# Performance work log

Hardware: AMD Instinct MI355X
Metric: run time of the kernel (lower is better)

The kernel has to match this reference:

```python
import jax, jax.numpy as jnp
import numpy as np

GOP = 4


def conv3x3(x, w, b):
    y = jax.lax.conv_general_dilated(x, w, (1, 1), 'SAME',
                                     dimension_numbers=('NCHW', 'OIHW', 'NCHW'))
    return y + b[None, :, None, None]


def resize_bilinear(x, oh, ow):
    # F.interpolate(mode='bilinear', align_corners=False), no antialias
    N, C, H, W = x.shape
    ys = (jnp.arange(oh, dtype=x.dtype) + 0.5) * (H / oh) - 0.5
    xs = (jnp.arange(ow, dtype=x.dtype) + 0.5) * (W / ow) - 0.5
    y0 = jnp.floor(ys); x0 = jnp.floor(xs)
    ty = (ys - y0)[:, None]; tx = (xs - x0)[None, :]
    y0i = jnp.clip(y0, 0, H - 1).astype(jnp.int32)
    y1i = jnp.clip(y0 + 1, 0, H - 1).astype(jnp.int32)
    x0i = jnp.clip(x0, 0, W - 1).astype(jnp.int32)
    x1i = jnp.clip(x0 + 1, 0, W - 1).astype(jnp.int32)
    r00 = x[:, :, y0i][:, :, :, x0i]; r01 = x[:, :, y0i][:, :, :, x1i]
    r10 = x[:, :, y1i][:, :, :, x0i]; r11 = x[:, :, y1i][:, :, :, x1i]
    top = r00 * (1 - tx) + r01 * tx
    bot = r10 * (1 - tx) + r11 * tx
    return top * (1 - ty) + bot * ty


def deform_sample_1x1(feat, off):
    # torchvision deform_conv2d with 1x1 kernel: bilinear gather at
    # (h + dy, w + dx), zero outside; offset channels are (dy, dx).
    N, C, H, W = feat.shape
    dy, dx = off[:, 0], off[:, 1]                       # [N,H,W]
    gy = jnp.arange(H, dtype=feat.dtype)[:, None] + dy  # [N,H,W]
    gx = jnp.arange(W, dtype=feat.dtype)[None, :] + dx
    y0 = jnp.floor(gy); x0 = jnp.floor(gx)
    ty = (gy - y0)[:, None]; tx = (gx - x0)[:, None]    # [N,1,H,W]

    def corner(yi, xi):
        valid = (yi >= 0) & (yi < H) & (xi >= 0) & (xi < W)
        yc = jnp.clip(yi, 0, H - 1).astype(jnp.int32)
        xc = jnp.clip(xi, 0, W - 1).astype(jnp.int32)
        v = jax.vmap(lambda f, y, x: f[:, y, x])(feat, yc, xc)  # [N,C,H,W]
        return v * valid[:, None].astype(feat.dtype)

    return (corner(y0, x0) * (1 - ty) * (1 - tx)
            + corner(y0, x0 + 1) * (1 - ty) * tx
            + corner(y0 + 1, x0) * ty * (1 - tx)
            + corner(y0 + 1, x0 + 1) * ty * tx)


def setup_inputs() -> dict:
    key = jax.random.key(0)
    ks = jax.random.split(key, 20)
    dim = 256
    f32 = jnp.float32

    def p(k, shape, s=0.05):
        return jax.random.normal(k, shape, dtype=f32) * s

    return {
        'imgs': jax.random.normal(ks[0], (2, 16, 3, 224, 224), dtype=f32),
        'i_features': jax.random.normal(ks[1], (8, dim, 56, 56), dtype=f32),
        'p_motions': jax.random.normal(ks[2], (2, 12, 2, 112, 112), dtype=f32),
        'dw': p(ks[3], (dim, dim)), 'db': p(ks[4], (dim,)),
        'mw1': p(ks[5], (dim, dim, 3, 3)), 'mb1': p(ks[6], (dim,)),
        'mw2': p(ks[7], (dim, dim, 3, 3)), 'mb2': p(ks[8], (dim,)),
        'mw3': p(ks[9], (dim, dim, 3, 3)), 'mb3': p(ks[10], (dim,)),
        'ew1': p(ks[11], (dim, 2, 3, 3)), 'eb1': p(ks[12], (dim,)),
        'ew2': p(ks[13], (dim, dim, 3, 3)), 'eb2': p(ks[14], (dim,)),
        'ew3': p(ks[15], (dim, dim, 3, 3)), 'eb3': p(ks[16], (dim,)),
        'ew4': p(ks[17], (dim, dim, 3, 3)), 'eb4': p(ks[18], (dim,)),
    }


def reference(imgs, i_features, p_motions, dw, db, mw1, mb1, mw2, mb2, mw3, mb3,
              ew1, eb1, ew2, eb2, ew3, eb3, ew4, eb4):
    B = imgs.shape[0]
    num_gop = imgs.shape[1] // GOP
    h, w = i_features.shape[-2], i_features.shape[-1]
    scale = h / imgs.shape[-1]  # static python float
    Tp = p_motions.shape[1]
    k = Tp // num_gop

    # flatten motions over (b t), resize to feature res, rescale magnitudes
    pm = p_motions.reshape(B * Tp, 2, p_motions.shape[-2], p_motions.shape[-1])
    pm = resize_bilinear(pm, h, w) * scale              # [(b n k), 2, h, w]

    emb = jax.nn.relu(conv3x3(pm, ew1, eb1))
    emb = jax.nn.relu(conv3x3(emb, ew2, eb2))
    emb = jax.nn.relu(conv3x3(emb, ew3, eb3))
    emb = jax.nn.relu(conv3x3(emb, ew4, eb4))

    # i_features expanded to one copy per P-frame: (b n) -> (b n k)
    feat = jnp.repeat(i_features, k, axis=0)
    sampled = deform_sample_1x1(feat, pm)
    pf = jnp.einsum('nchw,oc->nohw', sampled, dw) + db[None, :, None, None]

    pf = jax.nn.relu(conv3x3(pf, mw1, mb1))
    pf = jax.nn.relu(conv3x3(pf, mw2, mb2))
    pf = jax.nn.relu(conv3x3(pf, mw3, mb3))
    p2d = pf + emb                                      # [(b n k), c, h, w]

    # adaptive_avg_pool2d(1) + flatten(3)
    pooled = p2d.reshape(B, num_gop, k, -1, h, w).mean(axis=(-2, -1))  # [b,n,k,c]
    return pooled, p2d
```

## Files before the change

### kernel.cpp

```cpp
#include <hip/hip_runtime.h>

#define NPIX 3136
#define NN   24
#define CDIM 256

typedef __attribute__((ext_vector_type(8))) short short8v;
typedef __attribute__((ext_vector_type(4))) float float4v;

typedef __attribute__((address_space(1))) const void gvoid;
typedef __attribute__((address_space(3))) void lvoid;
static __device__ __forceinline__ void async_copy16(const void* g, void* l) {
    __builtin_amdgcn_global_load_lds((gvoid*)g, (lvoid*)l, 16, 0, 0);
}

static __device__ __forceinline__ unsigned short f2b(float f) {
    unsigned int u = __float_as_uint(f);
    u = (u + 0x7FFFu + ((u >> 16) & 1u)) >> 16;
    return (unsigned short)u;
}
static __device__ __forceinline__ float b2f(unsigned short h) {
    return __uint_as_float(((unsigned int)h) << 16);
}

__global__ __launch_bounds__(256) void resize_pm_kernel(
    const float* __restrict__ pmo, float* __restrict__ pm)
{
    int idx = blockIdx.x * 256 + threadIdx.x;
    if (idx >= NN * 2 * NPIX) return;
    int x = idx % 56, y = (idx / 56) % 56, nc = idx / NPIX;
    const float* src = pmo + (size_t)nc * 112 * 112 + (size_t)(2 * y) * 112 + 2 * x;
    pm[idx] = (src[0] + src[1] + src[112] + src[113]) * 0.0625f;
}

__global__ __launch_bounds__(256) void pack_all_kernel(
    const float* __restrict__ s0, const float* __restrict__ s1,
    const float* __restrict__ s2, const float* __restrict__ s3,
    const float* __restrict__ s4, const float* __restrict__ s5,
    const float* __restrict__ sdw, unsigned short* __restrict__ dstbase)
{
    int bx = blockIdx.x;
    if (bx < 6 * 2304) {
        int wi = bx / 2304;
        int d = (bx % 2304) * 256 + threadIdx.x;
        const float* w = (wi == 0) ? s0 : (wi == 1) ? s1 : (wi == 2) ? s2
                       : (wi == 3) ? s3 : (wi == 4) ? s4 : s5;
        int j = d & 7;
        int lane = (d >> 3) & 63;
        int co, ci, tap;
        if (wi == 5) {
            int g = (d >> 9) & 3;
            int e = d >> 11;
            tap = e % 9;
            int f = e / 9;
            int ch = f & 7, cb = f >> 3;
            co = cb * 64 + g * 16 + (lane & 15);
            ci = ch * 32 + (lane >> 4) * 8 + j;
        } else {
            int mi = (d >> 9) & 7;
            int e = d >> 12;
            tap = e % 9;
            int f = e / 9;
            int ch = f & 7, cb = f >> 3;
            co = cb * 128 + mi * 16 + (lane & 15);
            ci = ch * 32 + (lane >> 4) * 8 + j;
        }
        dstbase[(size_t)wi * 589824 + d] = f2b(w[((size_t)co * 256 + ci) * 9 + tap]);
    } else {
        int d = (bx - 6 * 2304) * 256 + threadIdx.x;
        int j = d & 7;
        int lane = (d >> 3) & 63;
        int mi = (d >> 9) & 7;
        int e = d >> 12;
        int ch = e & 7, cb = e >> 3;
        int co = cb * 128 + mi * 16 + (lane & 15);
        int ci = ch * 32 + (lane >> 4) * 8 + j;
        dstbase[(size_t)6 * 589824 + d] = f2b(sdw[(size_t)co * 256 + ci]);
    }
}

__global__ __launch_bounds__(256) void ew1_kernel(
    const float* __restrict__ pm, const float* __restrict__ w,
    const float* __restrict__ b, unsigned short* __restrict__ out)
{
    __shared__ float sT[8][18];
    __shared__ float sW1[256 * 19];
    int n = blockIdx.y;
    int pixbase = blockIdx.x * 8;
    int t = threadIdx.x;
    if (t < 144) {
        int p = t / 18, j = t % 18;
        int ci = j / 9, tap = j % 9;
        int pix = pixbase + p;
        int y = pix / 56, x = pix % 56;
        int yy = y + tap / 3 - 1, xx = x + tap % 3 - 1;
        float v = 0.f;
        if ((unsigned)yy < 56u && (unsigned)xx < 56u)
            v = pm[((size_t)n * 2 + ci) * NPIX + yy * 56 + xx];
        sT[p][j] = v;
    }
    for (int idx = t; idx < 4608; idx += 256) {
        int co = idx / 18, j = idx % 18;
        sW1[co * 19 + j] = w[idx];
    }
    __syncthreads();
    int co = t;
    float bias = b[co];
#pragma unroll
    for (int p = 0; p < 8; p++) {
        float acc = bias;
#pragma unroll
        for (int j = 0; j < 18; j++) acc += sT[p][j] * sW1[co * 19 + j];
        acc = fmaxf(acc, 0.f);
        out[((size_t)n * NPIX + pixbase + p) * 256 + co] = f2b(acc);
    }
}

template <int TAPS, bool RELU, bool HASB>
__global__ __launch_bounds__(512, 2) void conv8_mfma(
    const unsigned short* __restrict__ in,
    const unsigned short* __restrict__ wp,
    const float* __restrict__ bias,
    unsigned short* __restrict__ out,
    const unsigned short* __restrict__ inB,
    const unsigned short* __restrict__ wpB,
    const float* __restrict__ biasB,
    unsigned short* __restrict__ outB,
    int zsplit)
{
    constexpr int W_ITERS = TAPS * 8;
    constexpr int SIN_SHORTS = (TAPS == 9) ? 10 * 58 * 32 : 448 * 32;

    __shared__ unsigned short sIn[2 * SIN_SHORTS];
    __shared__ unsigned short sW[W_ITERS * 512];

    const int r0 = blockIdx.x * 8;
    if (r0 >= 56) return;
    const int tid = threadIdx.x;
    const int lane = tid & 63;
    const int wv = tid >> 6;
    const int mih = wv >> 2;
    const int wpx = wv & 3;
    const int col = lane & 15;
    const int quad = lane >> 4;
    const int cb = blockIdx.y;

    int n = blockIdx.z;
    const unsigned short* inP = in;
    const unsigned short* wpP = wp;
    const float* biasP = bias;
    unsigned short* outP = out;
    if (n >= zsplit) {
        n -= zsplit;
        inP = inB; wpP = wpB; biasP = biasB; outP = outB;
    }

    const unsigned short* inN = inP + (size_t)n * NPIX * 256;
    const unsigned short* wcb = wpP + (size_t)cb * 8 * W_ITERS * 512;

    int rowoff[7];
#pragma unroll
    for (int nj = 0; nj < 7; nj++) {
        int pxl = wpx * 112 + nj * 16 + col;
        if (TAPS == 9) {
            int yl = pxl / 56;
            rowoff[nj] = yl * 58 + (pxl - yl * 56);
        } else {
            rowoff[nj] = pxl;
        }
    }
    const int qoff = quad * 8;
    const int laneSrc = (lane >> 2) * 256 + (lane & 3) * 8;

    auto stageW = [&](int ch) {
        const unsigned short* wchunk = wcb + (size_t)ch * W_ITERS * 512;
#pragma unroll
        for (int it = wv; it < W_ITERS; it += 8)
            async_copy16(wchunk + it * 512 + lane * 8, sW + it * 512);
    };
    auto stageI = [&](int ch, int half) {
        const int c0 = ch * 32;
        unsigned short* dst = sIn + half * SIN_SHORTS;
        if (TAPS == 9) {
#pragma unroll
            for (int s = wv; s < 40; s += 8) {
                int ry = s >> 2, k = s & 3;
                int gy = r0 + ry - 1;
                if ((unsigned)gy < 56u && (k < 3 || lane < 32))
                    async_copy16(inN + (size_t)gy * 14336 + k * 4096 + c0 + laneSrc,
                                 dst + ry * 1856 + 32 + k * 512);
            }
        } else {
#pragma unroll
            for (int s = wv; s < 28; s += 8)
                async_copy16(inN + (size_t)r0 * 14336 + s * 4096 + c0 + laneSrc,
                             dst + s * 512);
        }
    };

    if (TAPS == 9) {
        for (int i = tid * 8; i < 2 * SIN_SHORTS; i += 512 * 8)
            *(int4*)(sIn + i) = (int4){0, 0, 0, 0};
        __syncthreads();
    }

    float4v acc[4][7];
#pragma unroll
    for (int mi = 0; mi < 4; mi++)
#pragma unroll
        for (int nj = 0; nj < 7; nj++) acc[mi][nj] = (float4v){0.f, 0.f, 0.f, 0.f};

    stageW(0);
    stageI(0, 0);

    for (int ch = 0; ch < 8; ch++) {
        __syncthreads();
        if (ch < 7) stageI(ch + 1, (ch + 1) & 1);
        const int iOff = (ch & 1) * SIN_SHORTS;
#pragma unroll
        for (int tap = 0; tap < TAPS; tap++) {
            const int coff = (TAPS == 9) ? ((tap / 3) * 58 + (tap % 3)) * 32 : 0;
            short8v a[4], b[7];
#pragma unroll
            for (int mi = 0; mi < 4; mi++)
                a[mi] = *(const short8v*)(sW + ((tap * 8 + mih * 4 + mi) * 64 + lane) * 8);
#pragma unroll
            for (int nj = 0; nj < 7; nj++)
                b[nj] = *(const short8v*)(sIn + iOff + rowoff[nj] * 32 + coff + qoff);
#pragma unroll
            for (int mi = 0; mi < 4; mi++)
#pragma unroll
                for (int nj = 0; nj < 7; nj++)
                    acc[mi][nj] = __builtin_amdgcn_mfma_f32_16x16x32_bf16(
                        a[mi], b[nj], acc[mi][nj], 0, 0, 0);
        }
        if (ch < 7) {
            __syncthreads();
            stageW(ch + 1);
        }
    }

    unsigned short* outT = outP + ((size_t)n * NPIX + r0 * 56 + wpx * 112) * 256
                         + cb * 128 + mih * 64;
#pragma unroll
    for (int mi = 0; mi < 4; mi++) {
        float4v bv = (float4v){0.f, 0.f, 0.f, 0.f};
        if (HASB) bv = *(const float4v*)(biasP + cb * 128 + mih * 64 + mi * 16 + quad * 4);
#pragma unroll
        for (int nj = 0; nj < 7; nj++) {
            float v0 = acc[mi][nj][0] + bv[0];
            float v1 = acc[mi][nj][1] + bv[1];
            float v2 = acc[mi][nj][2] + bv[2];
            float v3 = acc[mi][nj][3] + bv[3];
            if (RELU) {
                v0 = fmaxf(v0, 0.f); v1 = fmaxf(v1, 0.f);
                v2 = fmaxf(v2, 0.f); v3 = fmaxf(v3, 0.f);
            }
            uint2 pk;
            pk.x = (unsigned)f2b(v0) | ((unsigned)f2b(v1) << 16);
            pk.y = (unsigned)f2b(v2) | ((unsigned)f2b(v3) << 16);
            *(uint2*)(outT + ((size_t)(nj * 16 + col)) * 256 + mi * 16 + quad * 4) = pk;
        }
    }
}

template <int TAPS, bool RELU, bool HASB, bool FUSE>
__global__ __launch_bounds__(256, 2) void conv_mfma(
    const unsigned short* __restrict__ in,
    const unsigned short* __restrict__ wp,
    const float* __restrict__ bias,
    unsigned short* __restrict__ out,
    const unsigned short* __restrict__ inB,
    const unsigned short* __restrict__ wpB,
    const float* __restrict__ biasB,
    unsigned short* __restrict__ outB,
    int zsplit,
    const unsigned short* __restrict__ emb,
    float* __restrict__ dout)
{
    constexpr int W_ITERS = TAPS * 4;
    constexpr int SIN_SHORTS = (TAPS == 9) ? 10 * 58 * 32 : 448 * 32;

    __shared__ unsigned short sIn[SIN_SHORTS];
    __shared__ unsigned short sW[W_ITERS * 512];

    const int r0 = blockIdx.x * 8;
    if (r0 >= 56) return;
    const int tid = threadIdx.x;
    const int lane = tid & 63;
    const int wv = tid >> 6;
    const int col = lane & 15;
    const int quad = lane >> 4;
    const int cb = blockIdx.y;

    int n = blockIdx.z;
    const unsigned short* inP = in;
    const unsigned short* wpP = wp;
    const float* biasP = bias;
    unsigned short* outP = out;
    if (n >= zsplit) {
        n -= zsplit;
        inP = inB; wpP = wpB; biasP = biasB; outP = outB;
    }

    const unsigned short* inN = inP + (size_t)n * NPIX * 256;
    const unsigned short* wcb = wpP + (size_t)cb * 8 * W_ITERS * 512;

    int rowoff[7];
#pragma unroll
    for (int nj = 0; nj < 7; nj++) {
        int pxl = wv * 112 + nj * 16 + col;
        if (TAPS == 9) {
            int yl = pxl / 56;
            rowoff[nj] = yl * 58 + (pxl - yl * 56);
        } else {
            rowoff[nj] = pxl;
        }
    }
    const int qoff = quad * 8;
    const int laneSrc = (lane >> 2) * 256 + (lane & 3) * 8;

    if (TAPS == 9) {
        for (int i = tid * 8; i < SIN_SHORTS; i += 2048)
            *(int4*)(sIn + i) = (int4){0, 0, 0, 0};
    }

    float4v acc[4][7];
#pragma unroll
    for (int mi = 0; mi < 4; mi++)
#pragma unroll
        for (int nj = 0; nj < 7; nj++) acc[mi][nj] = (float4v){0.f, 0.f, 0.f, 0.f};

    for (int ch = 0; ch < 8; ch++) {
        const int c0 = ch * 32;
        __syncthreads();
        const unsigned short* wchunk = wcb + (size_t)ch * W_ITERS * 512;
#pragma unroll
        for (int it = wv; it < W_ITERS; it += 4)
            async_copy16(wchunk + it * 512 + lane * 8, sW + it * 512);
        if (TAPS == 9) {
#pragma unroll
            for (int ry = 0; ry < 10; ry++) {
                int k = (wv - ry) & 3;
                int gy = r0 + ry - 1;
                if ((unsigned)gy < 56u && (k < 3 || lane < 32))
                    async_copy16(inN + (size_t)gy * 14336 + k * 4096 + c0 + laneSrc,
                                 sIn + ry * 1856 + 32 + k * 512);
            }
        } else {
#pragma unroll
            for (int k = 0; k < 7; k++) {
                int it = wv + k * 4;
                async_copy16(inN + (size_t)r0 * 14336 + it * 4096 + c0 + laneSrc,
                             sIn + it * 512);
            }
        }
        __syncthreads();
#pragma unroll
        for (int tap = 0; tap < TAPS; tap++) {
            const int coff = (TAPS == 9) ? ((tap / 3) * 58 + (tap % 3)) * 32 : 0;
            short8v a[4], b[7];
#pragma unroll
            for (int mi = 0; mi < 4; mi++)
                a[mi] = *(const short8v*)(sW + ((tap * 4 + mi) * 64 + lane) * 8);
#pragma unroll
            for (int nj = 0; nj < 7; nj++)
                b[nj] = *(const short8v*)(sIn + rowoff[nj] * 32 + coff + qoff);
#pragma unroll
            for (int mi = 0; mi < 4; mi++)
#pragma unroll
                for (int nj = 0; nj < 7; nj++)
                    acc[mi][nj] = __builtin_amdgcn_mfma_f32_16x16x32_bf16(
                        a[mi], b[nj], acc[mi][nj], 0, 0, 0);
        }
    }

    if (!FUSE) {
        unsigned short* outT = outP + ((size_t)n * NPIX + r0 * 56 + wv * 112) * 256 + cb * 64;
#pragma unroll
        for (int mi = 0; mi < 4; mi++) {
            float4v bv = (float4v){0.f, 0.f, 0.f, 0.f};
            if (HASB) bv = *(const float4v*)(biasP + cb * 64 + mi * 16 + quad * 4);
#pragma unroll
            for (int nj = 0; nj < 7; nj++) {
                float v0 = acc[mi][nj][0] + bv[0];
                float v1 = acc[mi][nj][1] + bv[1];
                float v2 = acc[mi][nj][2] + bv[2];
                float v3 = acc[mi][nj][3] + bv[3];
                if (RELU) {
                    v0 = fmaxf(v0, 0.f); v1 = fmaxf(v1, 0.f);
                    v2 = fmaxf(v2, 0.f); v3 = fmaxf(v3, 0.f);
                }
                uint2 pk;
                pk.x = (unsigned)f2b(v0) | ((unsigned)f2b(v1) << 16);
                pk.y = (unsigned)f2b(v2) | ((unsigned)f2b(v3) << 16);
                *(uint2*)(outT + ((size_t)(nj * 16 + col)) * 256 + mi * 16 + quad * 4) = pk;
            }
        }
    } else {
        const int pixBase = r0 * 56 + wv * 112;
        float* p2d = dout + 6144 + (size_t)n * CDIM * NPIX;
        float sums[4][4];
#pragma unroll
        for (int mi = 0; mi < 4; mi++)
#pragma unroll
            for (int q = 0; q < 4; q++) sums[mi][q] = 0.f;
#pragma unroll
        for (int mi = 0; mi < 4; mi++) {
            float4v bv = *(const float4v*)(biasP + cb * 64 + mi * 16 + quad * 4);
            const int co0 = cb * 64 + mi * 16 + quad * 4;
#pragma unroll
            for (int nj = 0; nj < 7; nj++) {
                int pix = pixBase + nj * 16 + col;
                uint2 e = *(const uint2*)(emb + ((size_t)n * NPIX + pix) * 256 + co0);
                float v0 = fmaxf(acc[mi][nj][0] + bv[0], 0.f) + b2f((unsigned short)(e.x & 0xFFFF));
                float v1 = fmaxf(acc[mi][nj][1] + bv[1], 0.f) + b2f((unsigned short)(e.x >> 16));
                float v2 = fmaxf(acc[mi][nj][2] + bv[2], 0.f) + b2f((unsigned short)(e.y & 0xFFFF));
                float v3 = fmaxf(acc[mi][nj][3] + bv[3], 0.f) + b2f((unsigned short)(e.y >> 16));
                p2d[(size_t)(co0 + 0) * NPIX + pix] = v0;
                p2d[(size_t)(co0 + 1) * NPIX + pix] = v1;
                p2d[(size_t)(co0 + 2) * NPIX + pix] = v2;
                p2d[(size_t)(co0 + 3) * NPIX + pix] = v3;
                sums[mi][0] += v0; sums[mi][1] += v1;
                sums[mi][2] += v2; sums[mi][3] += v3;
            }
        }
#pragma unroll
        for (int mi = 0; mi < 4; mi++)
#pragma unroll
            for (int q = 0; q < 4; q++) {
                float s = sums[mi][q];
                s += __shfl_down(s, 8, 16);
                s += __shfl_down(s, 4, 16);
                s += __shfl_down(s, 2, 16);
                s += __shfl_down(s, 1, 16);
                if (col == 0)
                    atomicAdd(dout + n * CDIM + cb * 64 + mi * 16 + quad * 4 + q,
                              s * (1.f / 3136.f));
            }
    }
}

__global__ __launch_bounds__(256) void transpose_fI(
    const float* __restrict__ feat, unsigned short* __restrict__ dst)
{
    __shared__ float s[64][65];
    int fi = blockIdx.z;
    int p0 = blockIdx.x * 64;
    int c0 = blockIdx.y * 64;
    int t = threadIdx.x;
    int pl = t & 63, cq = t >> 6;
#pragma unroll
    for (int i = 0; i < 16; i++) {
        int c = cq + i * 4;
        s[pl][c] = feat[((size_t)fi * 256 + c0 + c) * NPIX + p0 + pl];
    }
    __syncthreads();
    int cl = t & 63, pq = t >> 6;
#pragma unroll
    for (int i = 0; i < 16; i++) {
        int p = pq + i * 4;
        dst[((size_t)fi * NPIX + p0 + p) * 256 + c0 + cl] = f2b(s[p][cl]);
    }
}

__global__ __launch_bounds__(256) void deform_kernel(
    const unsigned short* __restrict__ Z,
    const float* __restrict__ pm,
    const float* __restrict__ db,
    unsigned short* __restrict__ out)
{
    int n = blockIdx.y;
    int t = threadIdx.x;
    int pix = blockIdx.x * 8 + (t >> 5);
    int g = t & 31;
    int fi = n / 3;
    int y = pix / 56, x = pix % 56;
    float dy = pm[((size_t)n * 2 + 0) * NPIX + pix];
    float dx = pm[((size_t)n * 2 + 1) * NPIX + pix];
    float gy = (float)y + dy, gx = (float)x + dx;
    float y0f = floorf(gy), x0f = floorf(gx);
    float ty = gy - y0f, tx = gx - x0f;
    int y0 = (int)y0f, x0 = (int)x0f, y1 = y0 + 1, x1 = x0 + 1;
    bool vy0 = (unsigned)y0 < 56u, vy1 = (unsigned)y1 < 56u;
    bool vx0 = (unsigned)x0 < 56u, vx1 = (unsigned)x1 < 56u;
    float w00 = (1.f - ty) * (1.f - tx) * (vy0 && vx0 ? 1.f : 0.f);
    float w01 = (1.f - ty) * tx * (vy0 && vx1 ? 1.f : 0.f);
    float w10 = ty * (1.f - tx) * (vy1 && vx0 ? 1.f : 0.f);
    float w11 = ty * tx * (vy1 && vx1 ? 1.f : 0.f);
    int y0c = vy0 ? y0 : 0, y1c = vy1 ? y1 : 0;
    int x0c = vx0 ? x0 : 0, x1c = vx1 ? x1 : 0;
    const unsigned short* Zf = Z + (size_t)fi * NPIX * 256 + g * 8;
    const unsigned short* p00 = Zf + (size_t)(y0c * 56 + x0c) * 256;
    const unsigned short* p01 = Zf + (size_t)(y0c * 56 + x1c) * 256;
    const unsigned short* p10 = Zf + (size_t)(y1c * 56 + x0c) * 256;
    const unsigned short* p11 = Zf + (size_t)(y1c * 56 + x1c) * 256;
    unsigned short r[8];
#pragma unroll
    for (int j = 0; j < 8; j++) {
        float v = b2f(p00[j]) * w00 + b2f(p01[j]) * w01 +
                  b2f(p10[j]) * w10 + b2f(p11[j]) * w11;
        v += db[g * 8 + j];
        r[j] = f2b(v);
    }
    *(int4*)(out + ((size_t)n * NPIX + pix) * 256 + g * 8) = *(int4*)r;
}

extern "C" void kernel_launch(void* const* d_in, const int* in_sizes, int n_in,
                              void* d_out, int out_size, void* d_ws, size_t ws_size,
                              hipStream_t stream)
{
    const float* i_features = (const float*)d_in[1];
    const float* p_motions  = (const float*)d_in[2];
    const float* dw  = (const float*)d_in[3];
    const float* db  = (const float*)d_in[4];
    const float* mw1 = (const float*)d_in[5];
    const float* mb1 = (const float*)d_in[6];
    const float* mw2 = (const float*)d_in[7];
    const float* mb2 = (const float*)d_in[8];
    const float* mw3 = (const float*)d_in[9];
    const float* mb3 = (const float*)d_in[10];
    const float* ew1 = (const float*)d_in[11];
    const float* eb1 = (const float*)d_in[12];
    const float* ew2 = (const float*)d_in[13];
    const float* eb2 = (const float*)d_in[14];
    const float* ew3 = (const float*)d_in[15];
    const float* eb3 = (const float*)d_in[16];
    const float* ew4 = (const float*)d_in[17];
    const float* eb4 = (const float*)d_in[18];
    float* out = (float*)d_out;

    const size_t SZ_PM  = 602112;
    const size_t SZ_WPK = 7208960;
    const size_t SZ_ACT = 38535168;
    char* p = (char*)d_ws;
    float* pm = (float*)p;            p += SZ_PM;
    unsigned short* wpk = (unsigned short*)p;
    unsigned short* wpE2 = wpk + 0 * 589824;
    unsigned short* wpE3 = wpk + 1 * 589824;
    unsigned short* wpE4 = wpk + 2 * 589824;
    unsigned short* wpM1 = wpk + 3 * 589824;
    unsigned short* wpM2 = wpk + 4 * 589824;
    unsigned short* wpM3 = wpk + 5 * 589824;
    unsigned short* wpDW = wpk + 6 * 589824;
    p += SZ_WPK;
    unsigned short* bufA = (unsigned short*)p; p += SZ_ACT;
    unsigned short* bufB = (unsigned short*)p; p += SZ_ACT;
    unsigned short* bufC = (unsigned short*)p; p += SZ_ACT;
    unsigned short* bufD = (unsigned short*)p;

    const bool paired = ws_size >= SZ_PM + SZ_WPK + 4 * SZ_ACT;

    hipMemsetAsync(out, 0, 6144 * sizeof(float), stream);

    resize_pm_kernel<<<(NN * 2 * NPIX + 255) / 256, 256, 0, stream>>>(p_motions, pm);
    pack_all_kernel<<<6 * 2304 + 256, 256, 0, stream>>>(
        ew2, ew3, ew4, mw1, mw2, mw3, dw, wpk);

    dim3 cg24(8, 2, NN), cg48(8, 2, 2 * NN), cg8(8, 2, 8);
    dim3 cgF(8, 4, NN);

    if (paired) {
        ew1_kernel<<<dim3(392, NN), 256, 0, stream>>>(pm, ew1, eb1, bufA);
        conv8_mfma<9, true, true><<<cg24, 512, 0, stream>>>(
            bufA, wpE2, eb2, bufB,  bufA, wpE2, eb2, bufB, NN);
        unsigned short* fI = bufA;
        unsigned short* Zb = bufA + (size_t)8 * NPIX * 256;
        transpose_fI<<<dim3(49, 4, 8), 256, 0, stream>>>(i_features, fI);
        conv8_mfma<1, false, false><<<cg8, 512, 0, stream>>>(
            fI, wpDW, nullptr, Zb,  fI, wpDW, nullptr, Zb, NN);
        deform_kernel<<<dim3(392, NN), 256, 0, stream>>>(Zb, pm, db, bufC);
        conv8_mfma<9, true, true><<<cg48, 512, 0, stream>>>(
            bufB, wpE3, eb3, bufA,  bufC, wpM1, mb1, bufD, NN);
        conv8_mfma<9, true, true><<<cg48, 512, 0, stream>>>(
            bufA, wpE4, eb4, bufB,  bufD, wpM2, mb2, bufC, NN);
        conv_mfma<9, true, true, true><<<cgF, 256, 0, stream>>>(
            bufC, wpM3, mb3, nullptr,  bufC, wpM3, mb3, nullptr, NN, bufB, out);
    } else {
        ew1_kernel<<<dim3(392, NN), 256, 0, stream>>>(pm, ew1, eb1, bufA);
        conv8_mfma<9, true, true><<<cg24, 512, 0, stream>>>(
            bufA, wpE2, eb2, bufB,  bufA, wpE2, eb2, bufB, NN);
        conv8_mfma<9, true, true><<<cg24, 512, 0, stream>>>(
            bufB, wpE3, eb3, bufA,  bufB, wpE3, eb3, bufA, NN);
        conv8_mfma<9, true, true><<<cg24, 512, 0, stream>>>(
            bufA, wpE4, eb4, bufC,  bufA, wpE4, eb4, bufC, NN);
        transpose_fI<<<dim3(49, 4, 8), 256, 0, stream>>>(i_features, bufA);
        conv8_mfma<1, false, false><<<cg8, 512, 0, stream>>>(
            bufA, wpDW, nullptr, bufB,  bufA, wpDW, nullptr, bufB, NN);
        deform_kernel<<<dim3(392, NN), 256, 0, stream>>>(bufB, pm, db, bufA);
        conv8_mfma<9, true, true><<<cg24, 512, 0, stream>>>(
            bufA, wpM1, mb1, bufB,  bufA, wpM1, mb1, bufB, NN);
        conv8_mfma<9, true, true><<<cg24, 512, 0, stream>>>(
            bufB, wpM2, mb2, bufA,  bufB, wpM2, mb2, bufA, NN);
        conv_mfma<9, true, true, true><<<cgF, 256, 0, stream>>>(
            bufA, wpM3, mb3, nullptr,  bufA, wpM3, mb3, nullptr, NN, bufC, out);
    }
}
```

Before: 751.6 us.

## Add software-pipelined 3x3 conv kernel with split weight staging and async loads

Adds a new conv8p_mfma kernel for the 3x3 bf16 convolutions. It double-buffers the input tile and splits each channel chunk's weights into two LDS halves (taps 0-3 and 4-8), so the next chunk's weights and input load asynchronously while the current taps compute. Explicit vmcnt waits, barriers and s_setprio raise priority around the MFMA sections. The goal is to hide global-to-LDS latency behind compute, at the cost of more LDS use and a hand-tuned wait schedule that must match the number of issued copies exactly.

```diff
diff --git a/kernel.cpp b/kernel.cpp
--- a/kernel.cpp
+++ b/kernel.cpp
@@ -21,6 +21,12 @@
 static __device__ __forceinline__ float b2f(unsigned short h) {
     return __uint_as_float(((unsigned int)h) << 16);
 }
+
+#define WAIT_VMCNT(N) do { \
+    asm volatile("s_waitcnt vmcnt(" #N ")" ::: "memory"); \
+    __builtin_amdgcn_sched_barrier(0); } while (0)
+#define BARRIER() do { __builtin_amdgcn_s_barrier(); \
+    __builtin_amdgcn_sched_barrier(0); } while (0)
 
 __global__ __launch_bounds__(256) void resize_pm_kernel(
     const float* __restrict__ pmo, float* __restrict__ pm)
@@ -112,6 +118,182 @@
         for (int j = 0; j < 18; j++) acc += sT[p][j] * sW1[co * 19 + j];
         acc = fmaxf(acc, 0.f);
         out[((size_t)n * NPIX + pixbase + p) * 256 + co] = f2b(acc);
+    }
+}
+
+__global__ __launch_bounds__(512, 2) void conv8p_mfma(
+    const unsigned short* __restrict__ in,
+    const unsigned short* __restrict__ wp,
+    const float* __restrict__ bias,
+    unsigned short* __restrict__ out,
+    const unsigned short* __restrict__ inB,
+    const unsigned short* __restrict__ wpB,
+    const float* __restrict__ biasB,
+    unsigned short* __restrict__ outB,
+    int zsplit)
+{
+    constexpr int SIN_SHORTS = 10 * 58 * 32;
+
+    __shared__ unsigned short sIn[2 * SIN_SHORTS];
+    __shared__ unsigned short sWa[32 * 512];
+    __shared__ unsigned short sWb[40 * 512];
+    __shared__ unsigned short sTrash[512];
+
+    const int r0 = blockIdx.x * 8;
+    if (r0 >= 56) return;
+    const int tid = threadIdx.x;
+    const int lane = tid & 63;
+    const int wv = tid >> 6;
+    const int mih = wv >> 2;
+    const int wpx = wv & 3;
+    const int col = lane & 15;
+    const int quad = lane >> 4;
+    const int cb = blockIdx.y;
+
+    int n = blockIdx.z;
+    const unsigned short* inP = in;
+    const unsigned short* wpP = wp;
+    const float* biasP = bias;
+    unsigned short* outP = out;
+    if (n >= zsplit) {
+        n -= zsplit;
+        inP = inB; wpP = wpB; biasP = biasB; outP = outB;
+    }
+
+    const unsigned short* inN = inP + (size_t)n * NPIX * 256;
+    const unsigned short* wcb = wpP + (size_t)cb * 8 * 72 * 512;
+
+    int rowoff[7];
+#pragma unroll
+    for (int nj = 0; nj < 7; nj++) {
+        int pxl = wpx * 112 + nj * 16 + col;
+        int yl = pxl / 56;
+        rowoff[nj] = yl * 58 + (pxl - yl * 56);
+    }
+    const int qoff = quad * 8;
+    const int laneSrc = (lane >> 2) * 256 + (lane & 3) * 8;
+
+    auto stage_a = [&](int ch) {
+        const bool dummy = (ch > 7);
+        const unsigned short* wchunk = wcb + (size_t)(dummy ? 0 : ch) * 72 * 512;
+#pragma unroll
+        for (int i = 0; i < 4; i++) {
+            int it = wv + 8 * i;
+            async_copy16(wchunk + it * 512 + lane * 8,
+                         dummy ? (unsigned short*)sTrash : (sWa + it * 512));
+        }
+    };
+    auto stage_b = [&](int ch) {
+        const unsigned short* wchunk = wcb + (size_t)ch * 72 * 512;
+#pragma unroll
+        for (int i = 0; i < 5; i++) {
+            int it = 32 + wv + 8 * i;
+            async_copy16(wchunk + it * 512 + lane * 8, sWb + (it - 32) * 512);
+        }
+    };
+    auto stage_I = [&](int ch) {
+        const bool dummy = (ch > 7);
+        unsigned short* dst0 = sIn + (ch & 1) * SIN_SHORTS;
+        const int c0 = (dummy ? 0 : ch) * 32;
+#pragma unroll
+        for (int i = 0; i < 5; i++) {
+            int s = wv + 8 * i;
+            int ry = s >> 2, k = s & 3;
+            int gy = r0 + ry - 1;
+            bool valid = ((unsigned)gy < 56u) && !dummy;
+            const unsigned short* src =
+                inN + (size_t)(valid ? gy : 0) * 14336 + k * 4096 + c0 + laneSrc;
+            unsigned short* dst = valid ? (dst0 + ry * 1856 + 32 + k * 512)
+                                        : (unsigned short*)sTrash;
+            if (k < 3 || lane < 32)
+                async_copy16(src, dst);
+        }
+    };
+
+    for (int i = tid * 8; i < 2 * SIN_SHORTS; i += 512 * 8)
+        *(int4*)(sIn + i) = (int4){0, 0, 0, 0};
+    asm volatile("s_waitcnt lgkmcnt(0)" ::: "memory");
+    BARRIER();
+
+    float4v acc[4][7];
+#pragma unroll
+    for (int mi = 0; mi < 4; mi++)
+#pragma unroll
+        for (int nj = 0; nj < 7; nj++) acc[mi][nj] = (float4v){0.f, 0.f, 0.f, 0.f};
+
+    stage_I(0); stage_a(0); stage_I(1); stage_b(0);
+
+    for (int ch = 0; ch < 8; ch++) {
+        const int iOff = (ch & 1) * SIN_SHORTS;
+
+        WAIT_VMCNT(10);
+        BARRIER();
+        __builtin_amdgcn_s_setprio(1);
+#pragma unroll
+        for (int tap = 0; tap < 4; tap++) {
+            const int coff = ((tap / 3) * 58 + (tap % 3)) * 32;
+            short8v a[4], b[7];
+#pragma unroll
+            for (int mi = 0; mi < 4; mi++)
+                a[mi] = *(const short8v*)(sWa + ((tap * 8 + mih * 4 + mi) * 64 + lane) * 8);
+#pragma unroll
+            for (int nj = 0; nj < 7; nj++)
+                b[nj] = *(const short8v*)(sIn + iOff + rowoff[nj] * 32 + coff + qoff);
+#pragma unroll
+            for (int mi = 0; mi < 4; mi++)
+#pragma unroll
+                for (int nj = 0; nj < 7; nj++)
+                    acc[mi][nj] = __builtin_amdgcn_mfma_f32_16x16x32_bf16(
+                        a[mi], b[nj], acc[mi][nj], 0, 0, 0);
+        }
+        __builtin_amdgcn_s_setprio(0);
+        BARRIER();
+        stage_a(ch + 1);
+
+        WAIT_VMCNT(4);
+        BARRIER();
+        __builtin_amdgcn_s_setprio(1);
+#pragma unroll
+        for (int tap = 4; tap < 9; tap++) {
+            const int coff = ((tap / 3) * 58 + (tap % 3)) * 32;
+            short8v a[4], b[7];
+#pragma unroll
+            for (int mi = 0; mi < 4; mi++)
+                a[mi] = *(const short8v*)(sWb + (((tap - 4) * 8 + mih * 4 + mi) * 64 + lane) * 8);
+#pragma unroll
+            for (int nj = 0; nj < 7; nj++)
+                b[nj] = *(const short8v*)(sIn + iOff + rowoff[nj] * 32 + coff + qoff);
+#pragma unroll
+            for (int mi = 0; mi < 4; mi++)
+#pragma unroll
+                for (int nj = 0; nj < 7; nj++)
+                    acc[mi][nj] = __builtin_amdgcn_mfma_f32_16x16x32_bf16(
+                        a[mi], b[nj], acc[mi][nj], 0, 0, 0);
+        }
+        __builtin_amdgcn_s_setprio(0);
+        if (ch < 7) {
+            BARRIER();
+            stage_I(ch + 2);
+            stage_b(ch + 1);
+        }
+    }
+
+    unsigned short* outT = outP + ((size_t)n * NPIX + r0 * 56 + wpx * 112) * 256
+                         + cb * 128 + mih * 64;
+#pragma unroll
+    for (int mi = 0; mi < 4; mi++) {
+        float4v bv = *(const float4v*)(biasP + cb * 128 + mih * 64 + mi * 16 + quad * 4);
+#pragma unroll
+        for (int nj = 0; nj < 7; nj++) {
+            float v0 = fmaxf(acc[mi][nj][0] + bv[0], 0.f);
+            float v1 = fmaxf(acc[mi][nj][1] + bv[1], 0.f);
+            float v2 = fmaxf(acc[mi][nj][2] + bv[2], 0.f);
+            float v3 = fmaxf(acc[mi][nj][3] + bv[3], 0.f);
+            uint2 pk;
+            pk.x = (unsigned)f2b(v0) | ((unsigned)f2b(v1) << 16);
+            pk.y = (unsigned)f2b(v2) | ((unsigned)f2b(v3) << 16);
+            *(uint2*)(outT + ((size_t)(nj * 16 + col)) * 256 + mi * 16 + quad * 4) = pk;
+        }
     }
 }
 
@@ -561,7 +743,7 @@
 
     if (paired) {
         ew1_kernel<<<dim3(392, NN), 256, 0, stream>>>(pm, ew1, eb1, bufA);
-        conv8_mfma<9, true, true><<<cg24, 512, 0, stream>>>(
+        conv8p_mfma<<<cg24, 512, 0, stream>>>(
             bufA, wpE2, eb2, bufB,  bufA, wpE2, eb2, bufB, NN);
         unsigned short* fI = bufA;
         unsigned short* Zb = bufA + (size_t)8 * NPIX * 256;
@@ -569,27 +751,27 @@
         conv8_mfma<1, false, false><<<cg8, 512, 0, stream>>>(
             fI, wpDW, nullptr, Zb,  fI, wpDW, nullptr, Zb, NN);
         deform_kernel<<<dim3(392, NN), 256, 0, stream>>>(Zb, pm, db, bufC);
-        conv8_mfma<9, true, true><<<cg48, 512, 0, stream>>>(
+        conv8p_mfma<<<cg48, 512, 0, stream>>>(
             bufB, wpE3, eb3, bufA,  bufC, wpM1, mb1, bufD, NN);
-        conv8_mfma<9, true, true><<<cg48, 512, 0, stream>>>(
+        conv8p_mfma<<<cg48, 512, 0, stream>>>(
             bufA, wpE4, eb4, bufB,  bufD, wpM2, mb2, bufC, NN);
         conv_mfma<9, true, true, true><<<cgF, 256, 0, stream>>>(
             bufC, wpM3, mb3, nullptr,  bufC, wpM3, mb3, nullptr, NN, bufB, out);
     } else {
         ew1_kernel<<<dim3(392, NN), 256, 0, stream>>>(pm, ew1, eb1, bufA);
-        conv8_mfma<9, true, true><<<cg24, 512, 0, stream>>>(
+        conv8p_mfma<<<cg24, 512, 0, stream>>>(
             bufA, wpE2, eb2, bufB,  bufA, wpE2, eb2, bufB, NN);
-        conv8_mfma<9, true, true><<<cg24, 512, 0, stream>>>(
+        conv8p_mfma<<<cg24, 512, 0, stream>>>(
             bufB, wpE3, eb3, bufA,  bufB, wpE3, eb3, bufA, NN);
-        conv8_mfma<9, true, true><<<cg24, 512, 0, stream>>>(
+        conv8p_mfma<<<cg24, 512, 0, stream>>>(
             bufA, wpE4, eb4, bufC,  bufA, wpE4, eb4, bufC, NN);
         transpose_fI<<<dim3(49, 4, 8), 256, 0, stream>>>(i_features, bufA);
         conv8_mfma<1, false, false><<<cg8, 512, 0, stream>>>(
             bufA, wpDW, nullptr, bufB,  bufA, wpDW, nullptr, bufB, NN);
         deform_kernel<<<dim3(392, NN), 256, 0, stream>>>(bufB, pm, db, bufA);
-        conv8_mfma<9, true, true><<<cg24, 512, 0, stream>>>(
+        conv8p_mfma<<<cg24, 512, 0, stream>>>(
             bufA, wpM1, mb1, bufB,  bufA, wpM1, mb1, bufB, NN);
-        conv8_mfma<9, true, true><<<cg24, 512, 0, stream>>>(
+        conv8p_mfma<<<cg24, 512, 0, stream>>>(
             bufB, wpM2, mb2, bufA,  bufB, wpM2, mb2, bufA, NN);
         conv_mfma<9, true, true, true><<<cgF, 256, 0, stream>>>(
             bufA, wpM3, mb3, nullptr,  bufA, wpM3, mb3, nullptr, NN, bufC, out);
```

New measurement: 759.3 us. No clear change (+1.0%).
